# Performance work log

Hardware: AMD Instinct MI355X
Metric: run time of the kernel (lower is better)

The kernel has to match this reference:

```python
import jax, jax.numpy as jnp
import numpy as np

N = 100000   # nodes
E = 1600000  # edges
F = 256      # n_feats
H = 128      # n_hidden
HEADS = 8
C = 64       # n_class


def setup_inputs() -> dict:
    key = jax.random.key(0)
    ks = jax.random.split(key, 32)
    rn = lambda k, shape, s=0.05: jax.random.normal(k, shape, jnp.float32) * s
    return {
        'x': rn(ks[0], (N, F), 1.0),
        'src': jax.random.randint(ks[1], (E,), 0, N, jnp.int32),
        'dst': jax.random.randint(ks[2], (E,), 0, N, jnp.int32),
        'in_W': rn(ks[3], (F, H)), 'in_b': jnp.zeros((H,), jnp.float32),
        # layer 0 (concat=True, dim_out = H // HEADS)
        'q0_W': rn(ks[4], (H, H)), 'q0_b': jnp.zeros((H,), jnp.float32),
        'k0_W': rn(ks[5], (H, H)), 'k0_b': jnp.zeros((H,), jnp.float32),
        'v0_W': rn(ks[6], (H, H)), 'v0_b': jnp.zeros((H,), jnp.float32),
        'res0_W': rn(ks[7], (H, H)), 'res0_b': jnp.zeros((H,), jnp.float32),
        'gate0_W': rn(ks[8], (3 * H, 1)),
        'ln0_g': jnp.ones((H,), jnp.float32), 'ln0_b': jnp.zeros((H,), jnp.float32),
        # layer 1 (last: dim_out = C per head, concat=False, only_gate residual)
        'q1_W': rn(ks[9], (H, C * HEADS)), 'q1_b': jnp.zeros((C * HEADS,), jnp.float32),
        'k1_W': rn(ks[10], (H, C * HEADS)), 'k1_b': jnp.zeros((C * HEADS,), jnp.float32),
        'v1_W': rn(ks[11], (H, C * HEADS)), 'v1_b': jnp.zeros((C * HEADS,), jnp.float32),
        'res1_W': rn(ks[12], (H, C)), 'res1_b': jnp.zeros((C,), jnp.float32),
        'gate1_W': rn(ks[13], (3 * C, 1)),
    }


def _attn(x, qW, qb, kW, kb, vW, vb, src, dst, concat):
    n = x.shape[0]
    q = (x @ qW + qb).reshape(n, HEADS, -1)
    k = (x @ kW + kb).reshape(n, HEADS, -1)
    v = (x @ vW + vb).reshape(n, HEADS, -1)
    d = q.shape[-1]
    # u_dot_v: per-edge dot(q[src], k[dst]) -> [E, HEADS]
    s = jnp.einsum('ehd,ehd->eh', q[src], k[dst]) / jnp.sqrt(jnp.float32(d))
    # edge_softmax: segment softmax over incoming edges of each dst node
    m = jax.ops.segment_max(s, dst, num_segments=n)
    e = jnp.exp(s - m[dst])
    z = jax.ops.segment_sum(e, dst, num_segments=n)
    p = e / z[dst]
    # u_mul_e_sum: scatter-add v[src] * p to dst
    out = jax.ops.segment_sum(v[src] * p[:, :, None], dst, num_segments=n)
    return out.reshape(n, -1) if concat else out.mean(axis=1)


def _layernorm(x, g, b, eps=1e-5):
    mu = x.mean(-1, keepdims=True)
    var = ((x - mu) ** 2).mean(-1, keepdims=True)
    return (x - mu) / jnp.sqrt(var + eps) * g + b


def _gated_res(x, res, rW, rb, gW, ln_g=None, ln_b=None, only_gate=False):
    res = res @ rW + rb
    gate = jax.nn.sigmoid(jnp.concatenate([x, res, x - res], axis=-1) @ gW)
    out = x * gate + res * (1.0 - gate)
    if only_gate:
        return out
    return jax.nn.relu(_layernorm(out, ln_g, ln_b))


def reference(x, src, dst, in_W, in_b,
              q0_W, q0_b, k0_W, k0_b, v0_W, v0_b, res0_W, res0_b, gate0_W, ln0_g, ln0_b,
              q1_W, q1_b, k1_W, k1_b, v1_W, v1_b, res1_W, res1_b, gate1_W):
    h = x @ in_W + in_b
    a0 = _attn(h, q0_W, q0_b, k0_W, k0_b, v0_W, v0_b, src, dst, concat=True)
    h = _gated_res(a0, h, res0_W, res0_b, gate0_W, ln0_g, ln0_b, only_gate=False)
    a1 = _attn(h, q1_W, q1_b, k1_W, k1_b, v1_W, v1_b, src, dst, concat=False)
    out = _gated_res(a1, h, res1_W, res1_b, gate1_W, only_gate=True)
    return out
```

## Files before the change

### kernel.cpp

```cpp
#include <hip/hip_runtime.h>


typedef unsigned short u16;
typedef __attribute__((ext_vector_type(8))) unsigned short ushort8;
typedef __attribute__((ext_vector_type(8))) short short8v;
typedef __attribute__((ext_vector_type(4))) float f32x4;
typedef __attribute__((ext_vector_type(2))) float f32x2;

__device__ __forceinline__ float bf2f(unsigned short u) {
    return __uint_as_float(((unsigned)u) << 16);
}
__device__ __forceinline__ unsigned short f2bf(float f) {
    unsigned u = __float_as_uint(f);
    unsigned r = 0x7fffu + ((u >> 16) & 1u);
    return (unsigned short)((u + r) >> 16);
}
__device__ __forceinline__ unsigned char f2fp8(float f) {
    return (unsigned char)__builtin_amdgcn_cvt_pk_fp8_f32(f, 0.f, 0, false);
}

__device__ __forceinline__ void gload16(const void* gp, const void* lp) {
    __builtin_amdgcn_global_load_lds(
        (const __attribute__((address_space(1))) unsigned*)(uintptr_t)gp,
        (__attribute__((address_space(3))) unsigned*)(unsigned)(uintptr_t)lp,
        16, 0, 0);
}

__global__ void prep_k(const float* __restrict__ inW,
                       const float* __restrict__ q0W, const float* __restrict__ k0W,
                       const float* __restrict__ v0W, const float* __restrict__ r0W,
                       const float* __restrict__ q1W, const float* __restrict__ k1W,
                       const float* __restrict__ v1W, const float* __restrict__ r1W,
                       u16* __restrict__ arena) {
    int i = blockIdx.x * 256 + threadIdx.x;
    if (i >= 303104) return;
    float val;
    if (i < 32768) {
        int n = i >> 8, k = i & 255;
        val = inW[k * 128 + n];
    } else if (i < 81920) {
        int j = i - 32768;
        int r = j >> 7, kk = j & 127;
        int sec = r >> 7, c = r & 127;
        const float* s = (sec == 0) ? q0W : (sec == 1) ? k0W : v0W;
        val = s[kk * 128 + c];
    } else if (i < 98304) {
        int j = i - 81920;
        int r = j >> 7, kk = j & 127;
        val = r0W[kk * 128 + r];
    } else if (i < 294912) {
        int j = i - 98304;
        int row = j >> 7, kk = j & 127;
        int p = row / 768, rr = row - p * 768;
        int sec = rr >> 8, c = p * 256 + (rr & 255);
        const float* s = (sec == 0) ? q1W : (sec == 1) ? k1W : v1W;
        val = s[kk * 512 + c];
    } else {
        int j = i - 294912;
        int n = j >> 7, kk = j & 127;
        val = r1W[kk * 64 + n];
    }
    arena[i] = f2bf(val);
}

__global__ void bias_k(const float* __restrict__ q0b, const float* __restrict__ k0b,
                       const float* __restrict__ v0b, const float* __restrict__ r0b,
                       const float* __restrict__ q1b, const float* __restrict__ k1b,
                       const float* __restrict__ v1b, const float* __restrict__ r1b,
                       float* __restrict__ out) {
    int i = blockIdx.x * 256 + threadIdx.x;
    if (i >= 2112) return;
    if (i < 384) {
        int sec = i >> 7, c = i & 127;
        out[i] = (sec == 0) ? q0b[c] : (sec == 1) ? k0b[c] : v0b[c];
    } else if (i < 512) {
        out[i] = r0b[i - 384];
    } else if (i < 2048) {
        int j = i - 512;
        int p = j / 768, rr = j - p * 768;
        int sec = rr >> 8, c = p * 256 + (rr & 255);
        out[i] = (sec == 0) ? q1b[c] : (sec == 1) ? k1b[c] : v1b[c];
    } else {
        out[i] = r1b[i - 2048];
    }
}

__global__ void cvt_k(const float* __restrict__ in, u16* __restrict__ out, int n8) {
    int i = blockIdx.x * 256 + threadIdx.x;
    if (i >= n8) return;
    float4 a = *(const float4*)(in + (size_t)i * 8);
    float4 b = *(const float4*)(in + (size_t)i * 8 + 4);
    ushort8 o = {f2bf(a.x), f2bf(a.y), f2bf(a.z), f2bf(a.w),
                 f2bf(b.x), f2bf(b.y), f2bf(b.z), f2bf(b.w)};
    *(ushort8*)(out + (size_t)i * 8) = o;
}

template <int MODE, int K>
__global__ __launch_bounds__(256) void mgemm7(const u16* __restrict__ A,
                                              const u16* __restrict__ Bt,
                                              const float* __restrict__ bias,
                                              void* __restrict__ C,
                                              float* __restrict__ C2,
                                              int M, int MB, int ny, int Nvalid) {
    __shared__ __align__(16) unsigned char smem[36864];
    u16* As = (u16*)smem;
    u16* Bs = (u16*)(smem + 16384);
    int id = blockIdx.x;
    int xcd = id & 7, rest = id >> 3;
    int y = rest % ny;
    int x = (rest / ny) * 8 + xcd;
    if (x >= MB) return;
    const int bm = x * 128;
    const int bn = y * 128;
    const int t = threadIdx.x, lane = t & 63, wid = t >> 6;
    const int wm = (wid >> 1) * 64, wn = (wid & 1) * 64;
    const int jlog = ((lane & 7) ^ (lane >> 3)) * 8;
    f32x4 acc[4][4] = {};
    for (int k0 = 0; k0 < K; k0 += 64) {
#pragma unroll
        for (int c2 = 0; c2 < 4; ++c2) {
            int seg = c2 * 4 + wid;
            int row = seg * 8 + (lane >> 3);
            int ga = bm + row; if (ga >= M) ga = 0;
            gload16(A + (size_t)ga * K + k0 + jlog, (const char*)As + seg * 1024);
            int gb = bn + row; if (gb >= Nvalid) gb = 0;
            gload16(Bt + (size_t)gb * K + k0 + jlog, (const char*)Bs + seg * 1024);
        }
        __syncthreads();
#pragma unroll
        for (int ks = 0; ks < 2; ++ks) {
            const int jx = ks * 4 + (lane >> 4);
            short8v af[4], bfr[4];
#pragma unroll
            for (int i = 0; i < 4; ++i) {
                int ra = wm + i * 16 + (lane & 15);
                af[i] = *(const short8v*)((const char*)As + ra * 128 + ((jx ^ (ra & 7)) << 4));
                int rb = wn + i * 16 + (lane & 15);
                bfr[i] = *(const short8v*)((const char*)Bs + rb * 128 + ((jx ^ (rb & 7)) << 4));
            }
#pragma unroll
            for (int mi = 0; mi < 4; ++mi)
#pragma unroll
                for (int ni = 0; ni < 4; ++ni)
                    acc[mi][ni] = __builtin_amdgcn_mfma_f32_16x16x32_bf16(
                        af[mi], bfr[ni], acc[mi][ni], 0, 0, 0);
        }
        if (k0 + 64 < K) __syncthreads();
    }
    const int sec = y;
    bool fp8lds = false;
    int gsecoff = 0, rowbytes = 0;
    if (MODE == 1) {
        if (sec == 0)      { fp8lds = true; gsecoff = 0;   rowbytes = 512; }
        else if (sec == 2) { fp8lds = true; gsecoff = 384; rowbytes = 512; }
    } else if (MODE >= 2) {
        if (sec < 2)                  { fp8lds = true; gsecoff = sec * 128;             rowbytes = 1024; }
        else if (sec >= 4 && sec < 6) { fp8lds = true; gsecoff = 768 + (sec - 4) * 128; rowbytes = 1024; }
    }
    if (fp8lds) {
        unsigned char* tile = smem;
        __syncthreads();
#pragma unroll
        for (int ni = 0; ni < 4; ++ni) {
            int lcol = wn + ni * 16 + (lane & 15);
            float bs = bias[bn + lcol];
#pragma unroll
            for (int mi = 0; mi < 4; ++mi) {
#pragma unroll
                for (int j = 0; j < 4; ++j) {
                    int lrow = wm + mi * 16 + (lane >> 4) * 4 + j;
                    float val = acc[mi][ni][j] + bs;
                    tile[lrow * 144 + ((((lcol >> 4) ^ (lrow & 7)) << 4) | (lcol & 15))] =
                        f2fp8(val * 16.f);
                }
            }
        }
        __syncthreads();
#pragma unroll
        for (int it = 0; it < 4; ++it) {
            int lin = it * 256 + t;
            int row = lin >> 3, ch = lin & 7;
            int crow = bm + row;
            if (crow < M) {
                const float4 vsrc = *(const float4*)(tile + row * 144 + ((ch ^ (row & 7)) << 4));
                *(float4*)((unsigned char*)C + (size_t)crow * rowbytes + gsecoff + ch * 16) = vsrc;
            }
        }
        return;
    }
    bool bf16lds = false;
    if (MODE == 0)                         { bf16lds = true; gsecoff = 0;   rowbytes = 256; }
    else if (MODE == 1 && sec == 1)        { bf16lds = true; gsecoff = 128; rowbytes = 512; }
    else if (MODE >= 2 && sec >= 2 && sec < 4) {
        bf16lds = true; gsecoff = 256 + (sec - 2) * 256; rowbytes = 1024;
    }
    if (bf16lds) {
        unsigned char* tile = smem;
        __syncthreads();
#pragma unroll
        for (int ni = 0; ni < 4; ++ni) {
            int lcol = wn + ni * 16 + (lane & 15);
            float bs = bias[bn + lcol];
            int by = lcol * 2, ch = by >> 4;
#pragma unroll
            for (int mi = 0; mi < 4; ++mi) {
#pragma unroll
                for (int j = 0; j < 4; ++j) {
                    int lrow = wm + mi * 16 + (lane >> 4) * 4 + j;
                    float val = acc[mi][ni][j] + bs;
                    *(u16*)(tile + lrow * 272 + ((ch ^ (lrow & 7)) << 4) + (by & 15)) = f2bf(val);
                }
            }
        }
        __syncthreads();
#pragma unroll
        for (int it = 0; it < 8; ++it) {
            int lin = it * 256 + t;
            int row = lin >> 4, ch = lin & 15;
            int crow = bm + row;
            if (crow < M) {
                const float4 vsrc = *(const float4*)(tile + row * 272 + ((ch ^ (row & 7)) << 4));
                *(float4*)((unsigned char*)C + (size_t)crow * rowbytes + gsecoff + ch * 16) = vsrc;
            }
        }
        return;
    }
#pragma unroll
    for (int ni = 0; ni < 4; ++ni) {
        int lcol = wn + ni * 16 + (lane & 15);
        int ccol = bn + lcol;
        if (ccol >= Nvalid) continue;
        float bs = bias[ccol];
#pragma unroll
        for (int mi = 0; mi < 4; ++mi) {
#pragma unroll
            for (int j = 0; j < 4; ++j) {
                int crow = bm + wm + mi * 16 + (lane >> 4) * 4 + j;
                if (crow >= M) continue;
                float val = acc[mi][ni][j] + bs;
                if (MODE == 1) {
                    C2[(size_t)crow * 128 + lcol] = val;
                } else {
                    C2[(size_t)crow * 64 + lcol] = val;
                }
            }
        }
    }
}

__global__ void zero2_k(int* __restrict__ a, int* __restrict__ b, int n) {
    int i = blockIdx.x * 256 + threadIdx.x;
    if (i < n) { a[i] = 0; b[i] = 0; }
}

__global__ void hist_k(const int* __restrict__ dst, int* __restrict__ cnt, int E) {
    int i = blockIdx.x * 256 + threadIdx.x;
    if (i < E) atomicAdd(&cnt[dst[i]], 1);
}

__global__ void blocksum_k(const int* __restrict__ cnt, int* __restrict__ bsum, int n) {
    __shared__ int sd[256];
    int i = blockIdx.x * 256 + threadIdx.x;
    sd[threadIdx.x] = (i < n) ? cnt[i] : 0;
    __syncthreads();
    for (int off = 128; off > 0; off >>= 1) {
        if (threadIdx.x < off) sd[threadIdx.x] += sd[threadIdx.x + off];
        __syncthreads();
    }
    if (threadIdx.x == 0) bsum[blockIdx.x] = sd[0];
}

__global__ void scanb_k(int* bsum, int nb) {
    __shared__ int tmp[512];
    int t = threadIdx.x;
    tmp[t] = (t < nb) ? bsum[t] : 0;
    __syncthreads();
    for (int off = 1; off < 512; off <<= 1) {
        int v = (t >= off) ? tmp[t - off] : 0;
        __syncthreads();
        tmp[t] += v;
        __syncthreads();
    }
    if (t < nb) bsum[t] = (t ? tmp[t - 1] : 0);
}

__global__ void scanc_k(const int* __restrict__ cnt, const int* __restrict__ bsum,
                        int* __restrict__ row_off, int n, int E) {
    __shared__ int tmp[256];
    int b = blockIdx.x, t = threadIdx.x;
    int i = b * 256 + t;
    int own = (i < n) ? cnt[i] : 0;
    tmp[t] = own;
    __syncthreads();
    for (int off = 1; off < 256; off <<= 1) {
        int v = (t >= off) ? tmp[t - off] : 0;
        __syncthreads();
        tmp[t] += v;
        __syncthreads();
    }
    if (i < n) row_off[i] = bsum[b] + tmp[t] - own;
    if (b == 0 && t == 0) row_off[n] = E;
}

__global__ void scatter_k(const int* __restrict__ src, const int* __restrict__ dst,
                          const int* __restrict__ row_off, int* __restrict__ cur,
                          int* __restrict__ csr_src, int E) {
    int i = blockIdx.x * 256 + threadIdx.x;
    if (i < E) {
        int d = dst[i];
        int pos = row_off[d] + atomicAdd(&cur[d], 1);
        csr_src[pos] = src[i];
    }
}

__global__ __launch_bounds__(256) void attn0_k(const unsigned char* __restrict__ qkv,
                                               const int* __restrict__ row_off,
                                               const int* __restrict__ csr,
                                               float* __restrict__ out, int n) {
    int w = (blockIdx.x * 256 + threadIdx.x) >> 6;
    int lane = threadIdx.x & 63;
    if (w >= n) return;
    int beg = row_off[w], end = row_off[w + 1];
    unsigned kv = *(const unsigned*)(qkv + (size_t)w * 512 + 128 + 4 * lane);
    const float KS = 0.25f / 16.f;
    float k0f = bf2f((u16)kv) * KS, k1f = bf2f((u16)(kv >> 16)) * KS;
    float den = 0.f, num0 = 0.f, num1 = 0.f;
    int e = beg;
    for (; e + 4 <= end; e += 4) {
        int s0 = csr[e], s1 = csr[e + 1], s2 = csr[e + 2], s3 = csr[e + 3];
        const unsigned char* r0 = qkv + (size_t)s0 * 512;
        const unsigned char* r1 = qkv + (size_t)s1 * 512;
        const unsigned char* r2 = qkv + (size_t)s2 * 512;
        const unsigned char* r3 = qkv + (size_t)s3 * 512;
        int qa = *(const unsigned short*)(r0 + 2 * lane);
        int qb = *(const unsigned short*)(r1 + 2 * lane);
        int qc = *(const unsigned short*)(r2 + 2 * lane);
        int qd = *(const unsigned short*)(r3 + 2 * lane);
        int va = *(const unsigned short*)(r0 + 384 + 2 * lane);
        int vb = *(const unsigned short*)(r1 + 384 + 2 * lane);
        int vc = *(const unsigned short*)(r2 + 384 + 2 * lane);
        int vd = *(const unsigned short*)(r3 + 384 + 2 * lane);
        f32x2 qaf = __builtin_amdgcn_cvt_pk_f32_fp8(qa, false);
        f32x2 qbf = __builtin_amdgcn_cvt_pk_f32_fp8(qb, false);
        f32x2 qcf = __builtin_amdgcn_cvt_pk_f32_fp8(qc, false);
        f32x2 qdf = __builtin_amdgcn_cvt_pk_f32_fp8(qd, false);
        float pa = qaf.x * k0f + qaf.y * k1f;
        float pb = qbf.x * k0f + qbf.y * k1f;
        float pc = qcf.x * k0f + qcf.y * k1f;
        float pd = qdf.x * k0f + qdf.y * k1f;
#pragma unroll
        for (int off = 1; off < 8; off <<= 1) {
            pa += __shfl_xor(pa, off); pb += __shfl_xor(pb, off);
            pc += __shfl_xor(pc, off); pd += __shfl_xor(pd, off);
        }
        float wa = __expf(pa), wb = __expf(pb);
        float wc = __expf(pc), wd = __expf(pd);
        den += (wa + wb) + (wc + wd);
        f32x2 vaf = __builtin_amdgcn_cvt_pk_f32_fp8(va, false);
        f32x2 vbf = __builtin_amdgcn_cvt_pk_f32_fp8(vb, false);
        f32x2 vcf = __builtin_amdgcn_cvt_pk_f32_fp8(vc, false);
        f32x2 vdf = __builtin_amdgcn_cvt_pk_f32_fp8(vd, false);
        num0 = fmaf(wa, vaf.x, num0); num1 = fmaf(wa, vaf.y, num1);
        num0 = fmaf(wb, vbf.x, num0); num1 = fmaf(wb, vbf.y, num1);
        num0 = fmaf(wc, vcf.x, num0); num1 = fmaf(wc, vcf.y, num1);
        num0 = fmaf(wd, vdf.x, num0); num1 = fmaf(wd, vdf.y, num1);
    }
    for (; e < end; ++e) {
        int s = csr[e];
        const unsigned char* r = qkv + (size_t)s * 512;
        int qv = *(const unsigned short*)(r + 2 * lane);
        f32x2 qf = __builtin_amdgcn_cvt_pk_f32_fp8(qv, false);
        float p = qf.x * k0f + qf.y * k1f;
        p += __shfl_xor(p, 1);
        p += __shfl_xor(p, 2);
        p += __shfl_xor(p, 4);
        float wt = __expf(p);
        den += wt;
        int vv = *(const unsigned short*)(r + 384 + 2 * lane);
        f32x2 vf = __builtin_amdgcn_cvt_pk_f32_fp8(vv, false);
        num0 = fmaf(wt, vf.x, num0); num1 = fmaf(wt, vf.y, num1);
    }
    float inv = (end > beg) ? (1.f / den) * (1.f / 16.f) : 0.f;
    *(float2*)(out + ((size_t)w << 7) + 2 * lane) = make_float2(num0 * inv, num1 * inv);
}

template <bool FIRST>
__global__ __launch_bounds__(256) void attn1f_k(const unsigned char* __restrict__ qkv,
                                                const int* __restrict__ row_off,
                                                const int* __restrict__ csr,
                                                float* __restrict__ out, int n) {
    int w = (blockIdx.x * 256 + threadIdx.x) >> 6;
    int lane = threadIdx.x & 63;
    if (w >= n) return;
    int beg = row_off[w], end = row_off[w + 1];
    const float KS = 0.125f / 16.f;
    float kr0, kr1, kr2, kr3;
    {
        uint2 kk2 = *(const uint2*)(qkv + (size_t)w * 1024 + 256 + 8 * lane);
        kr0 = bf2f((u16)kk2.x) * KS; kr1 = bf2f((u16)(kk2.x >> 16)) * KS;
        kr2 = bf2f((u16)kk2.y) * KS; kr3 = bf2f((u16)(kk2.y >> 16)) * KS;
    }
    float den = 0.f, num0 = 0.f, num1 = 0.f, num2 = 0.f, num3 = 0.f;
    int e = beg;
    for (; e + 4 <= end; e += 4) {
        int s0 = csr[e], s1 = csr[e + 1], s2 = csr[e + 2], s3 = csr[e + 3];
        const unsigned char* r0 = qkv + (size_t)s0 * 1024;
        const unsigned char* r1 = qkv + (size_t)s1 * 1024;
        const unsigned char* r2 = qkv + (size_t)s2 * 1024;
        const unsigned char* r3 = qkv + (size_t)s3 * 1024;
        unsigned qa = *(const unsigned*)(r0 + 4 * lane);
        unsigned qb = *(const unsigned*)(r1 + 4 * lane);
        unsigned qc = *(const unsigned*)(r2 + 4 * lane);
        unsigned qd = *(const unsigned*)(r3 + 4 * lane);
        unsigned va = *(const unsigned*)(r0 + 768 + 4 * lane);
        unsigned vb = *(const unsigned*)(r1 + 768 + 4 * lane);
        unsigned vc = *(const unsigned*)(r2 + 768 + 4 * lane);
        unsigned vd = *(const unsigned*)(r3 + 768 + 4 * lane);
        f32x2 qa0 = __builtin_amdgcn_cvt_pk_f32_fp8((int)qa, false);
        f32x2 qa1 = __builtin_amdgcn_cvt_pk_f32_fp8((int)qa, true);
        f32x2 qb0 = __builtin_amdgcn_cvt_pk_f32_fp8((int)qb, false);
        f32x2 qb1 = __builtin_amdgcn_cvt_pk_f32_fp8((int)qb, true);
        f32x2 qc0 = __builtin_amdgcn_cvt_pk_f32_fp8((int)qc, false);
        f32x2 qc1 = __builtin_amdgcn_cvt_pk_f32_fp8((int)qc, true);
        f32x2 qd0 = __builtin_amdgcn_cvt_pk_f32_fp8((int)qd, false);
        f32x2 qd1 = __builtin_amdgcn_cvt_pk_f32_fp8((int)qd, true);
        float pa = qa0.x * kr0 + qa0.y * kr1 + qa1.x * kr2 + qa1.y * kr3;
        float pb = qb0.x * kr0 + qb0.y * kr1 + qb1.x * kr2 + qb1.y * kr3;
        float pc = qc0.x * kr0 + qc0.y * kr1 + qc1.x * kr2 + qc1.y * kr3;
        float pd = qd0.x * kr0 + qd0.y * kr1 + qd1.x * kr2 + qd1.y * kr3;
#pragma unroll
        for (int off = 1; off < 16; off <<= 1) {
            pa += __shfl_xor(pa, off); pb += __shfl_xor(pb, off);
            pc += __shfl_xor(pc, off); pd += __shfl_xor(pd, off);
        }
        float wa = __expf(pa), wb = __expf(pb);
        float wc = __expf(pc), wd = __expf(pd);
        den += (wa + wb) + (wc + wd);
        f32x2 va0 = __builtin_amdgcn_cvt_pk_f32_fp8((int)va, false);
        f32x2 va1 = __builtin_amdgcn_cvt_pk_f32_fp8((int)va, true);
        f32x2 vb0 = __builtin_amdgcn_cvt_pk_f32_fp8((int)vb, false);
        f32x2 vb1 = __builtin_amdgcn_cvt_pk_f32_fp8((int)vb, true);
        f32x2 vc0 = __builtin_amdgcn_cvt_pk_f32_fp8((int)vc, false);
        f32x2 vc1 = __builtin_amdgcn_cvt_pk_f32_fp8((int)vc, true);
        f32x2 vd0 = __builtin_amdgcn_cvt_pk_f32_fp8((int)vd, false);
        f32x2 vd1 = __builtin_amdgcn_cvt_pk_f32_fp8((int)vd, true);
        num0 = fmaf(wa, va0.x, num0); num1 = fmaf(wa, va0.y, num1);
        num2 = fmaf(wa, va1.x, num2); num3 = fmaf(wa, va1.y, num3);
        num0 = fmaf(wb, vb0.x, num0); num1 = fmaf(wb, vb0.y, num1);
        num2 = fmaf(wb, vb1.x, num2); num3 = fmaf(wb, vb1.y, num3);
        num0 = fmaf(wc, vc0.x, num0); num1 = fmaf(wc, vc0.y, num1);
        num2 = fmaf(wc, vc1.x, num2); num3 = fmaf(wc, vc1.y, num3);
        num0 = fmaf(wd, vd0.x, num0); num1 = fmaf(wd, vd0.y, num1);
        num2 = fmaf(wd, vd1.x, num2); num3 = fmaf(wd, vd1.y, num3);
    }
    for (; e < end; ++e) {
        int s = csr[e];
        const unsigned char* r = qkv + (size_t)s * 1024;
        unsigned qv = *(const unsigned*)(r + 4 * lane);
        f32x2 q0 = __builtin_amdgcn_cvt_pk_f32_fp8((int)qv, false);
        f32x2 q1 = __builtin_amdgcn_cvt_pk_f32_fp8((int)qv, true);
        float p = q0.x * kr0 + q0.y * kr1 + q1.x * kr2 + q1.y * kr3;
#pragma unroll
        for (int off = 1; off < 16; off <<= 1) p += __shfl_xor(p, off);
        float wt = __expf(p);
        den += wt;
        unsigned vv = *(const unsigned*)(r + 768 + 4 * lane);
        f32x2 v0 = __builtin_amdgcn_cvt_pk_f32_fp8((int)vv, false);
        f32x2 v1 = __builtin_amdgcn_cvt_pk_f32_fp8((int)vv, true);
        num0 = fmaf(wt, v0.x, num0); num1 = fmaf(wt, v0.y, num1);
        num2 = fmaf(wt, v1.x, num2); num3 = fmaf(wt, v1.y, num3);
    }
    float inv = (end > beg) ? 1.f / den : 0.f;
    float o0 = num0 * inv, o1 = num1 * inv, o2 = num2 * inv, o3 = num3 * inv;
    o0 += __shfl_xor(o0, 16); o1 += __shfl_xor(o1, 16);
    o2 += __shfl_xor(o2, 16); o3 += __shfl_xor(o3, 16);
    o0 += __shfl_xor(o0, 32); o1 += __shfl_xor(o1, 32);
    o2 += __shfl_xor(o2, 32); o3 += __shfl_xor(o3, 32);
    if (lane < 16) {
        const float HS = 1.f / 128.f;
        float4* op = (float4*)(out + ((size_t)w << 6) + lane * 4);
        if (FIRST) {
            *op = make_float4(o0 * HS, o1 * HS, o2 * HS, o3 * HS);
        } else {
            float4 tv = *op;
            tv.x += o0 * HS; tv.y += o1 * HS; tv.z += o2 * HS; tv.w += o3 * HS;
            *op = tv;
        }
    }
}

__global__ __launch_bounds__(256) void gres0_k(const float* __restrict__ x, const float* __restrict__ res,
                                               const float* __restrict__ gw,
                                               const float* __restrict__ lng, const float* __restrict__ lnb,
                                               u16* __restrict__ h1, int n) {
    int w = (blockIdx.x * 256 + threadIdx.x) >> 6;
    int lane = threadIdx.x & 63;
    if (w >= n) return;
    size_t base = (size_t)w * 128;
    float x1 = x[base + lane], x2 = x[base + lane + 64];
    float r1 = res[base + lane], r2 = res[base + lane + 64];
    float ca1 = gw[lane] + gw[256 + lane];
    float ca2 = gw[lane + 64] + gw[256 + lane + 64];
    float cr1 = gw[128 + lane] - gw[256 + lane];
    float cr2 = gw[128 + lane + 64] - gw[256 + lane + 64];
    float dot = x1 * ca1 + x2 * ca2 + r1 * cr1 + r2 * cr2;
#pragma unroll
    for (int off = 1; off < 64; off <<= 1) dot += __shfl_xor(dot, off);
    float g = 1.f / (1.f + __expf(-dot));
    float o1 = x1 * g + r1 * (1.f - g);
    float o2 = x2 * g + r2 * (1.f - g);
    float s = o1 + o2;
#pragma unroll
    for (int off = 1; off < 64; off <<= 1) s += __shfl_xor(s, off);
    float mu = s * (1.f / 128.f);
    float d1 = o1 - mu, d2 = o2 - mu;
    float vs = d1 * d1 + d2 * d2;
#pragma unroll
    for (int off = 1; off < 64; off <<= 1) vs += __shfl_xor(vs, off);
    float rstd = rsqrtf(vs * (1.f / 128.f) + 1e-5f);
    float y1 = d1 * rstd * lng[lane] + lnb[lane];
    float y2 = d2 * rstd * lng[lane + 64] + lnb[lane + 64];
    h1[base + lane] = f2bf(fmaxf(y1, 0.f));
    h1[base + lane + 64] = f2bf(fmaxf(y2, 0.f));
}

__global__ __launch_bounds__(256) void gres1_k(const float* __restrict__ x, const float* __restrict__ res,
                                               const float* __restrict__ gw,
                                               float* __restrict__ out, int n) {
    int w = (blockIdx.x * 256 + threadIdx.x) >> 6;
    int lane = threadIdx.x & 63;
    if (w >= n) return;
    size_t base = (size_t)w * 64;
    float xv = x[base + lane];
    float rv = res[base + lane];
    float ca = gw[lane] + gw[128 + lane];
    float cr = gw[64 + lane] - gw[128 + lane];
    float dot = xv * ca + rv * cr;
#pragma unroll
    for (int off = 1; off < 64; off <<= 1) dot += __shfl_xor(dot, off);
    float g = 1.f / (1.f + __expf(-dot));
    out[base + lane] = xv * g + rv * (1.f - g);
}

extern "C" void kernel_launch(void* const* d_in, const int* in_sizes, int n_in,
                              void* d_out, int out_size, void* d_ws, size_t ws_size,
                              hipStream_t stream) {
    const float* x    = (const float*)d_in[0];
    const int*   src  = (const int*)d_in[1];
    const int*   dst  = (const int*)d_in[2];
    const float* in_W = (const float*)d_in[3];
    const float* in_b = (const float*)d_in[4];
    const float* q0W = (const float*)d_in[5];  const float* q0b = (const float*)d_in[6];
    const float* k0W = (const float*)d_in[7];  const float* k0b = (const float*)d_in[8];
    const float* v0W = (const float*)d_in[9];  const float* v0b = (const float*)d_in[10];
    const float* r0W = (const float*)d_in[11]; const float* r0b = (const float*)d_in[12];
    const float* g0W = (const float*)d_in[13];
    const float* ln0g = (const float*)d_in[14]; const float* ln0b = (const float*)d_in[15];
    const float* q1W = (const float*)d_in[16]; const float* q1b = (const float*)d_in[17];
    const float* k1W = (const float*)d_in[18]; const float* k1b = (const float*)d_in[19];
    const float* v1W = (const float*)d_in[20]; const float* v1b = (const float*)d_in[21];
    const float* r1W = (const float*)d_in[22]; const float* r1b = (const float*)d_in[23];
    const float* g1W = (const float*)d_in[24];

    const int N = in_sizes[0] / 256;
    const int E = in_sizes[1];
    (void)ws_size; (void)n_in; (void)out_size;

    auto rnd = [](size_t b) { return (b + 255) & ~(size_t)255; };
    char* base = (char*)d_ws;
    const size_t S_bf = rnd((size_t)N * 128 * 2);
    const size_t S_f  = rnd((size_t)N * 128 * 4);
    size_t o = 0;
    int* row_off = (int*)(base + o); o += rnd(((size_t)N + 1) * 4);
    int* csr     = (int*)(base + o); o += rnd((size_t)E * 4);
    u16* warena  = (u16*)(base + o); o += rnd((size_t)303104 * 2);
    float* barena = (float*)(base + o); o += rnd((size_t)2112 * 4);
    const size_t R0 = o;
    const size_t R1 = R0 + S_f;
    const size_t R2 = R1 + 3 * S_bf;
    int* cnt  = (int*)(base + R0);
    int* cur  = (int*)(base + R0 + rnd((size_t)N * 4));
    int* bsum = (int*)(base + R0 + 2 * rnd((size_t)N * 4));
    u16*   h     = (u16*)(base + R0);
    float* a0    = (float*)(base + R0);
    float* res1o = (float*)(base + R0);
    float* a1    = (float*)(base + R0 + rnd((size_t)N * 64 * 4));
    u16* x_bf = (u16*)(base + R1);
    unsigned char* QKV0 = (unsigned char*)(base + R1);
    u16* h1   = (u16*)(base + R1);
    unsigned char* PASS = (unsigned char*)(base + R1 + S_bf);
    float* res0o = (float*)(base + R2);

    u16* inWt   = warena;
    u16* qkv0t  = warena + 32768;
    u16* qkv1t0 = warena + 98304;
    u16* qkv1t1 = warena + 196608;

    dim3 blk(256);
    int nwb = (N * 64 + 255) / 256;
    int nb  = (N + 255) / 256;
    int mb  = (N + 127) / 128;
    int xch = (mb + 7) / 8;

    prep_k<<<(303104 + 255) / 256, blk, 0, stream>>>(in_W, q0W, k0W, v0W, r0W,
                                                     q1W, k1W, v1W, r1W, warena);
    bias_k<<<9, blk, 0, stream>>>(q0b, k0b, v0b, r0b, q1b, k1b, v1b, r1b, barena);
    cvt_k<<<(N * 32 + 255) / 256, blk, 0, stream>>>(x, x_bf, N * 32);

    zero2_k<<<nb, blk, 0, stream>>>(cnt, cur, N);
    hist_k<<<(E + 255) / 256, blk, 0, stream>>>(dst, cnt, E);
    blocksum_k<<<nb, blk, 0, stream>>>(cnt, bsum, N);
    scanb_k<<<1, 512, 0, stream>>>(bsum, nb);
    scanc_k<<<nb, blk, 0, stream>>>(cnt, bsum, row_off, N, E);
    scatter_k<<<(E + 255) / 256, blk, 0, stream>>>(src, dst, row_off, cur, csr, E);

    mgemm7<0, 256><<<8 * 1 * xch, blk, 0, stream>>>(x_bf, inWt, in_b, h, nullptr,
                                                    N, mb, 1, 128);
    mgemm7<1, 128><<<8 * 4 * xch, blk, 0, stream>>>(h, qkv0t, barena, QKV0, res0o,
                                                    N, mb, 4, 512);
    attn0_k<<<nwb, blk, 0, stream>>>(QKV0, row_off, csr, a0, N);
    gres0_k<<<nwb, blk, 0, stream>>>(a0, res0o, g0W, ln0g, ln0b, h1, N);

    mgemm7<2, 128><<<8 * 6 * xch, blk, 0, stream>>>(h1, qkv1t0, barena + 512, PASS,
                                                    nullptr, N, mb, 6, 768);
    attn1f_k<true><<<nwb, blk, 0, stream>>>(PASS, row_off, csr, a1, N);

    mgemm7<3, 128><<<8 * 7 * xch, blk, 0, stream>>>(h1, qkv1t1, barena + 1280, PASS,
                                                    res1o, N, mb, 7, 832);
    attn1f_k<false><<<nwb, blk, 0, stream>>>(PASS, row_off, csr, a1, N);

    gres1_k<<<nwb, blk, 0, stream>>>(a1, res1o, g1W, (float*)d_out, N);
}
```

Baseline: 773.8 us.

## Fold input projection into layer-0 QKV/res weights and reuse histogram ranks

```diff
diff --git a/kernel.cpp b/kernel.cpp
--- a/kernel.cpp
+++ b/kernel.cpp
@@ -32,23 +32,10 @@
                        const float* __restrict__ q1W, const float* __restrict__ k1W,
                        const float* __restrict__ v1W, const float* __restrict__ r1W,
                        u16* __restrict__ arena) {
-    int i = blockIdx.x * 256 + threadIdx.x;
+    int i = blockIdx.x * 256 + threadIdx.x + 98304;
     if (i >= 303104) return;
     float val;
-    if (i < 32768) {
-        int n = i >> 8, k = i & 255;
-        val = inW[k * 128 + n];
-    } else if (i < 81920) {
-        int j = i - 32768;
-        int r = j >> 7, kk = j & 127;
-        int sec = r >> 7, c = r & 127;
-        const float* s = (sec == 0) ? q0W : (sec == 1) ? k0W : v0W;
-        val = s[kk * 128 + c];
-    } else if (i < 98304) {
-        int j = i - 81920;
-        int r = j >> 7, kk = j & 127;
-        val = r0W[kk * 128 + r];
-    } else if (i < 294912) {
+    if (i < 294912) {
         int j = i - 98304;
         int row = j >> 7, kk = j & 127;
         int p = row / 768, rr = row - p * 768;
@@ -63,25 +50,42 @@
     arena[i] = f2bf(val);
 }
 
-__global__ void bias_k(const float* __restrict__ q0b, const float* __restrict__ k0b,
-                       const float* __restrict__ v0b, const float* __restrict__ r0b,
-                       const float* __restrict__ q1b, const float* __restrict__ k1b,
+__global__ void cw_k(const float* __restrict__ inW, const float* __restrict__ in_b,
+                     const float* __restrict__ q0W, const float* __restrict__ k0W,
+                     const float* __restrict__ v0W, const float* __restrict__ r0W,
+                     const float* __restrict__ q0b, const float* __restrict__ k0b,
+                     const float* __restrict__ v0b, const float* __restrict__ r0b,
+                     u16* __restrict__ cwt, float* __restrict__ cwb) {
+    int i = blockIdx.x * 256 + threadIdx.x;
+    if (i < 131072) {
+        int n = i >> 8, k = i & 255;
+        int sec = n >> 7, c = n & 127;
+        const float* s = (sec == 0) ? q0W : (sec == 1) ? k0W : (sec == 2) ? v0W : r0W;
+        float acc = 0.f;
+        for (int j = 0; j < 128; ++j) acc = fmaf(inW[k * 128 + j], s[j * 128 + c], acc);
+        cwt[(size_t)n * 256 + k] = f2bf(acc);
+    } else if (i < 131584) {
+        int n = i - 131072;
+        int sec = n >> 7, c = n & 127;
+        const float* s = (sec == 0) ? q0W : (sec == 1) ? k0W : (sec == 2) ? v0W : r0W;
+        const float* b = (sec == 0) ? q0b : (sec == 1) ? k0b : (sec == 2) ? v0b : r0b;
+        float acc = b[c];
+        for (int j = 0; j < 128; ++j) acc = fmaf(in_b[j], s[j * 128 + c], acc);
+        cwb[n] = acc;
+    }
+}
+
+__global__ void bias_k(const float* __restrict__ q1b, const float* __restrict__ k1b,
                        const float* __restrict__ v1b, const float* __restrict__ r1b,
                        float* __restrict__ out) {
     int i = blockIdx.x * 256 + threadIdx.x;
-    if (i >= 2112) return;
-    if (i < 384) {
-        int sec = i >> 7, c = i & 127;
-        out[i] = (sec == 0) ? q0b[c] : (sec == 1) ? k0b[c] : v0b[c];
-    } else if (i < 512) {
-        out[i] = r0b[i - 384];
-    } else if (i < 2048) {
-        int j = i - 512;
-        int p = j / 768, rr = j - p * 768;
+    if (i >= 1600) return;
+    if (i < 1536) {
+        int p = i / 768, rr = i - p * 768;
         int sec = rr >> 8, c = p * 256 + (rr & 255);
         out[i] = (sec == 0) ? q1b[c] : (sec == 1) ? k1b[c] : v1b[c];
     } else {
-        out[i] = r1b[i - 2048];
+        out[i] = r1b[i - 1536];
     }
 }
 
@@ -189,8 +193,7 @@
         return;
     }
     bool bf16lds = false;
-    if (MODE == 0)                         { bf16lds = true; gsecoff = 0;   rowbytes = 256; }
-    else if (MODE == 1 && sec == 1)        { bf16lds = true; gsecoff = 128; rowbytes = 512; }
+    if (MODE == 1 && sec == 1)             { bf16lds = true; gsecoff = 128; rowbytes = 512; }
     else if (MODE >= 2 && sec >= 2 && sec < 4) {
         bf16lds = true; gsecoff = 256 + (sec - 2) * 256; rowbytes = 1024;
     }
@@ -248,14 +251,15 @@
     }
 }
 
-__global__ void zero2_k(int* __restrict__ a, int* __restrict__ b, int n) {
+__global__ void zero1_k(int* __restrict__ a, int n) {
     int i = blockIdx.x * 256 + threadIdx.x;
-    if (i < n) { a[i] = 0; b[i] = 0; }
-}
-
-__global__ void hist_k(const int* __restrict__ dst, int* __restrict__ cnt, int E) {
+    if (i < n) a[i] = 0;
+}
+
+__global__ void hist_k(const int* __restrict__ dst, int* __restrict__ cnt,
+                       int* __restrict__ rank, int E) {
     int i = blockIdx.x * 256 + threadIdx.x;
-    if (i < E) atomicAdd(&cnt[dst[i]], 1);
+    if (i < E) rank[i] = atomicAdd(&cnt[dst[i]], 1);
 }
 
 __global__ void blocksum_k(const int* __restrict__ cnt, int* __restrict__ bsum, int n) {
@@ -303,14 +307,10 @@
 }
 
 __global__ void scatter_k(const int* __restrict__ src, const int* __restrict__ dst,
-                          const int* __restrict__ row_off, int* __restrict__ cur,
+                          const int* __restrict__ row_off, const int* __restrict__ rank,
                           int* __restrict__ csr_src, int E) {
     int i = blockIdx.x * 256 + threadIdx.x;
-    if (i < E) {
-        int d = dst[i];
-        int pos = row_off[d] + atomicAdd(&cur[d], 1);
-        csr_src[pos] = src[i];
-    }
+    if (i < E) csr_src[row_off[dst[i]] + rank[i]] = src[i];
 }
 
 __global__ __launch_bounds__(256) void attn0_k(const unsigned char* __restrict__ qkv,
@@ -568,33 +568,30 @@
 
     auto rnd = [](size_t b) { return (b + 255) & ~(size_t)255; };
     char* base = (char*)d_ws;
-    const size_t S_bf = rnd((size_t)N * 128 * 2);
-    const size_t S_f  = rnd((size_t)N * 128 * 4);
+    const size_t S_f = rnd((size_t)N * 128 * 4);
     size_t o = 0;
     int* row_off = (int*)(base + o); o += rnd(((size_t)N + 1) * 4);
     int* csr     = (int*)(base + o); o += rnd((size_t)E * 4);
-    u16* warena  = (u16*)(base + o); o += rnd((size_t)303104 * 2);
-    float* barena = (float*)(base + o); o += rnd((size_t)2112 * 4);
-    const size_t R0 = o;
-    const size_t R1 = R0 + S_f;
-    const size_t R2 = R1 + 3 * S_bf;
-    int* cnt  = (int*)(base + R0);
-    int* cur  = (int*)(base + R0 + rnd((size_t)N * 4));
-    int* bsum = (int*)(base + R0 + 2 * rnd((size_t)N * 4));
-    u16*   h     = (u16*)(base + R0);
-    float* a0    = (float*)(base + R0);
-    float* res1o = (float*)(base + R0);
-    float* a1    = (float*)(base + R0 + rnd((size_t)N * 64 * 4));
-    u16* x_bf = (u16*)(base + R1);
-    unsigned char* QKV0 = (unsigned char*)(base + R1);
-    u16* h1   = (u16*)(base + R1);
-    unsigned char* PASS = (unsigned char*)(base + R1 + S_bf);
-    float* res0o = (float*)(base + R2);
-
-    u16* inWt   = warena;
-    u16* qkv0t  = warena + 32768;
+    u16* warena  = (u16*)(base + o); o += rnd((size_t)(303104 + 131072) * 2);
+    float* barena = (float*)(base + o); o += rnd((size_t)(1600 + 512) * 4);
+    char* RB = base + o;
+    int* cnt  = (int*)RB;
+    int* bsum = (int*)(RB + rnd((size_t)N * 4));
+    unsigned char* QKV0 = (unsigned char*)RB;
+    unsigned char* PASS = (unsigned char*)RB;
+    float* res0o = (float*)(RB + S_f);
+    u16*   x_bf  = (u16*)(RB + 2 * S_f);
+    float* a0    = (float*)(RB + 2 * S_f);
+    float* a1    = (float*)(RB + 2 * S_f);
+    float* res1o = (float*)(RB + 2 * S_f + rnd((size_t)N * 64 * 4));
+    int*   rank  = (int*)(RB + 3 * S_f);
+    u16*   h1    = (u16*)(RB + 3 * S_f);
+
     u16* qkv1t0 = warena + 98304;
     u16* qkv1t1 = warena + 196608;
+    u16* cwt    = warena + 303104;
+    float* qkv1b = barena;
+    float* cwb   = barena + 1600;
 
     dim3 blk(256);
     int nwb = (N * 64 + 255) / 256;
@@ -602,30 +599,30 @@
     int mb  = (N + 127) / 128;
     int xch = (mb + 7) / 8;
 
-    prep_k<<<(303104 + 255) / 256, blk, 0, stream>>>(in_W, q0W, k0W, v0W, r0W,
-                                                     q1W, k1W, v1W, r1W, warena);
-    bias_k<<<9, blk, 0, stream>>>(q0b, k0b, v0b, r0b, q1b, k1b, v1b, r1b, barena);
+    prep_k<<<(303104 - 98304 + 255) / 256, blk, 0, stream>>>(in_W, q0W, k0W, v0W, r0W,
+                                                             q1W, k1W, v1W, r1W, warena);
+    cw_k<<<(131584 + 255) / 256, blk, 0, stream>>>(in_W, in_b, q0W, k0W, v0W, r0W,
+                                                   q0b, k0b, v0b, r0b, cwt, cwb);
+    bias_k<<<7, blk, 0, stream>>>(q1b, k1b, v1b, r1b, barena);
     cvt_k<<<(N * 32 + 255) / 256, blk, 0, stream>>>(x, x_bf, N * 32);
 
-    zero2_k<<<nb, blk, 0, stream>>>(cnt, cur, N);
-    hist_k<<<(E + 255) / 256, blk, 0, stream>>>(dst, cnt, E);
+    zero1_k<<<nb, blk, 0, stream>>>(cnt, N);
+    hist_k<<<(E + 255) / 256, blk, 0, stream>>>(dst, cnt, rank, E);
     blocksum_k<<<nb, blk, 0, stream>>>(cnt, bsum, N);
     scanb_k<<<1, 512, 0, stream>>>(bsum, nb);
     scanc_k<<<nb, blk, 0, stream>>>(cnt, bsum, row_off, N, E);
-    scatter_k<<<(E + 255) / 256, blk, 0, stream>>>(src, dst, row_off, cur, csr, E);
-
-    mgemm7<0, 256><<<8 * 1 * xch, blk, 0, stream>>>(x_bf, inWt, in_b, h, nullptr,
-                                                    N, mb, 1, 128);
-    mgemm7<1, 128><<<8 * 4 * xch, blk, 0, stream>>>(h, qkv0t, barena, QKV0, res0o,
+    scatter_k<<<(E + 255) / 256, blk, 0, stream>>>(src, dst, row_off, rank, csr, E);
+
+    mgemm7<1, 256><<<8 * 4 * xch, blk, 0, stream>>>(x_bf, cwt, cwb, QKV0, res0o,
                                                     N, mb, 4, 512);
     attn0_k<<<nwb, blk, 0, stream>>>(QKV0, row_off, csr, a0, N);
     gres0_k<<<nwb, blk, 0, stream>>>(a0, res0o, g0W, ln0g, ln0b, h1, N);
 
-    mgemm7<2, 128><<<8 * 6 * xch, blk, 0, stream>>>(h1, qkv1t0, barena + 512, PASS,
+    mgemm7<2, 128><<<8 * 6 * xch, blk, 0, stream>>>(h1, qkv1t0, qkv1b, PASS,
                                                     nullptr, N, mb, 6, 768);
     attn1f_k<true><<<nwb, blk, 0, stream>>>(PASS, row_off, csr, a1, N);
 
-    mgemm7<3, 128><<<8 * 7 * xch, blk, 0, stream>>>(h1, qkv1t1, barena + 1280, PASS,
+    mgemm7<3, 128><<<8 * 7 * xch, blk, 0, stream>>>(h1, qkv1t1, qkv1b + 768, PASS,
                                                     res1o, N, mb, 7, 832);
     attn1f_k<false><<<nwb, blk, 0, stream>>>(PASS, row_off, csr, a1, N);
 
```

Result: faster. 739.3 us (-4.5%).
